# Kernel optimization log

Hardware: AMD Instinct MI355X
Metric: run time of the kernel (lower is better)

## Reference

```python
import jax, jax.numpy as jnp
import numpy as np

N, DIN, E, BLK = 16384, 128, 262144, 2048
H1, DH1, H2, DH2 = 4, 128, 4, 128
D, L, HT, OUT = 128, 5, 4, 2


def _gat(h_in, src, dst, W, a_s, a_d, b, concat):
    # PyG GATConv (eval mode, no dropout): message src->dst, softmax per dst
    H, Dh = a_s.shape
    h = (h_in @ W).reshape(N, H, Dh)
    als = jnp.einsum('nhd,hd->nh', h, a_s)
    ald = jnp.einsum('nhd,hd->nh', h, a_d)
    e = jax.nn.leaky_relu(als[src] + ald[dst], 0.2)            # [E2,H]
    m = jax.ops.segment_max(e, dst, num_segments=N)
    ex = jnp.exp(e - m[dst])
    den = jax.ops.segment_sum(ex, dst, num_segments=N)
    alpha = ex / (den[dst] + 1e-16)
    out = jax.ops.segment_sum(alpha[:, :, None] * h[src], dst, num_segments=N)
    return (out.reshape(N, H * Dh) if concat else out.mean(axis=1)) + b


def _pe():
    pos = jnp.arange(L, dtype=jnp.float32)[:, None]
    div = jnp.exp(jnp.arange(0, D, 2, dtype=jnp.float32) * (-jnp.log(10000.0) / D))
    return jnp.zeros((L, D)).at[:, 0::2].set(jnp.sin(pos * div)).at[:, 1::2].set(jnp.cos(pos * div))


def reference(x, edge_index, time_step, W1, a_src1, a_dst1, b1, W2, a_src2, a_dst2, b2,
              wq, bq, wk, bk, wv, bv, wo, bo, ln_g, ln_b, f1, fb1, f2, fb2, wc, bc):
    s, d = edge_index[0], edge_index[1]
    loops = jnp.arange(N, dtype=edge_index.dtype)
    src = jnp.concatenate([s, d, loops])
    dst = jnp.concatenate([d, s, loops])

    # structural encoder (two GAT layers)
    h = jax.nn.elu(_gat(x, src, dst, W1, a_src1, a_dst1, b1, True))
    h2 = _gat(h, src, dst, W2, a_src2, a_dst2, b2, False)       # [N, D]

    # temporal self-attention: banks are empty (one snapshot per node), so
    # seq has only the last slot valid; original detaches seq before temporal.
    seq = jnp.zeros((N, L, D), h2.dtype).at[:, L - 1].set(jax.lax.stop_gradient(h2))
    xs = seq + _pe()[None]                                       # [N,L,D]
    dh = D // HT
    q = xs[:, -1]                                                # only last query is used
    Q = (q @ wq + bq).reshape(N, HT, dh)
    K = (xs @ wk + bk).reshape(N, L, HT, dh)
    V = (xs @ wv + bv).reshape(N, L, HT, dh)
    scores = jnp.einsum('nhd,nlhd->nhl', Q, K) / jnp.sqrt(jnp.float32(dh))
    valid = (jnp.arange(L) == L - 1)                             # key_padding_mask: pad except last
    scores = jnp.where(valid[None, None, :], scores, -1e9)
    attn = jax.nn.softmax(scores, axis=-1)
    ctx = jnp.einsum('nhl,nlhd->nhd', attn, V).reshape(N, D)
    ao = ctx @ wo + bo

    def ln(v):
        mu = v.mean(-1, keepdims=True)
        var = v.var(-1, keepdims=True)
        return (v - mu) / jnp.sqrt(var + 1e-5) * ln_g + ln_b

    y = ln(q + ao)
    y = ln(y + jax.nn.relu(y @ f1 + fb1) @ f2 + fb2)
    return y @ wc + bc                                           # [N, 2]


def setup_inputs():
    key = jax.random.key(0)
    ks = jax.random.split(key, 20)
    src = jax.random.randint(ks[0], (E,), 0, N, dtype=jnp.int32)
    off = jax.random.randint(ks[1], (E,), 0, BLK, dtype=jnp.int32)
    dst = (src // BLK) * BLK + off                               # within-snapshot edges
    r = lambda k, shape, s=0.05: jax.random.normal(k, shape, jnp.float32) * s
    return {
        'x': jax.random.normal(ks[2], (N, DIN), jnp.float32),
        'edge_index': jnp.stack([src, dst]),
        'time_step': (jnp.arange(N) // BLK).astype(jnp.int64),
        'W1': r(ks[3], (DIN, H1 * DH1)), 'a_src1': r(ks[4], (H1, DH1)), 'a_dst1': r(ks[5], (H1, DH1)), 'b1': jnp.zeros((H1 * DH1,)),
        'W2': r(ks[6], (H1 * DH1, H2 * DH2)), 'a_src2': r(ks[7], (H2, DH2)), 'a_dst2': r(ks[8], (H2, DH2)), 'b2': jnp.zeros((DH2,)),
        'wq': r(ks[9], (D, D)), 'bq': jnp.zeros((D,)), 'wk': r(ks[10], (D, D)), 'bk': jnp.zeros((D,)),
        'wv': r(ks[11], (D, D)), 'bv': jnp.zeros((D,)), 'wo': r(ks[12], (D, D)), 'bo': jnp.zeros((D,)),
        'ln_g': jnp.ones((D,)), 'ln_b': jnp.zeros((D,)),
        'f1': r(ks[13], (D, 4 * D)), 'fb1': jnp.zeros((4 * D,)), 'f2': r(ks[14], (4 * D, D)), 'fb2': jnp.zeros((D,)),
        'wc': r(ks[15], (D, OUT)), 'bc': jnp.zeros((OUT,)),
    }
```

## Files before the change

kernel.cpp:

```cpp
#include <hip/hip_runtime.h>
#include <hip/hip_bf16.h>

#define NODES 16384
#define FEAT 512
typedef __hip_bfloat16 bf16;
typedef __hip_bfloat162 bf162;
typedef short short8v __attribute__((ext_vector_type(8)));
typedef float f32x4 __attribute__((ext_vector_type(4)));

static __device__ __forceinline__ float b2f(short s){
  return __uint_as_float(((unsigned)(unsigned short)s) << 16);
}
static __device__ __forceinline__ void split_store(bf16* h, bf16* l, size_t i, float v){
  bf16 hi = __float2bfloat16(v);
  h[i] = hi; l[i] = __float2bfloat16(v - __bfloat162float(hi));
}

__global__ void sentinel_kernel(float* __restrict__ out, int n, float v){
  int i = blockIdx.x*blockDim.x + threadIdx.x;
  if (i < n) out[i] = v;
}

__global__ void zero_kernel(int* __restrict__ p, int n){
  int i = blockIdx.x*blockDim.x + threadIdx.x;
  if (i < n) p[i] = 0;
}
__global__ void count_kernel(const int* __restrict__ ei, int* __restrict__ counts, int E){
  int i = blockIdx.x*blockDim.x + threadIdx.x;
  if (i < 2*E){
    int dst = (i < E) ? ei[E+i] : ei[i-E];
    atomicAdd(&counts[dst], 1);
  }
}
__global__ __launch_bounds__(1024) void scan_kernel(const int* __restrict__ counts,
                                                    int* __restrict__ offs, int* __restrict__ cursor){
  __shared__ int sh[1024];
  const int t = threadIdx.x;
  int loc[16]; int s = 0;
#pragma unroll
  for (int i=0;i<16;i++){ loc[i] = counts[t*16+i]; s += loc[i]; }
  sh[t] = s; __syncthreads();
  for (int d=1; d<1024; d<<=1){
    int v = (t>=d) ? sh[t-d] : 0;
    __syncthreads(); sh[t] += v; __syncthreads();
  }
  int run = (t==0) ? 0 : sh[t-1];
#pragma unroll
  for (int i=0;i<16;i++){ offs[t*16+i] = run; cursor[t*16+i] = run; run += loc[i]; }
  if (t==1023) offs[NODES] = run;
}
__global__ void fill_kernel(const int* __restrict__ ei, int* __restrict__ cursor,
                            unsigned short* __restrict__ csr, int E){
  int i = blockIdx.x*blockDim.x + threadIdx.x;
  if (i < 2*E){
    int src = ei[i];
    int dst = (i < E) ? ei[E+i] : ei[i-E];
    int pos = atomicAdd(&cursor[dst], 1);
    csr[pos] = (unsigned short)src;
  }
}

struct PrepArgs {
  const float *x,*W1,*W2,*wv,*wo,*f1,*f2;
  bf16 *xh,*w1h,*w2h,*wvh,*wvl,*woh,*wol,*f1h,*f1l,*f2h,*f2l;
};
__global__ __launch_bounds__(256) void prep_kernel(PrepArgs P){
  const int b = blockIdx.x;
  const int t = threadIdx.x;
  if (b < 512){
    const size_t base = (size_t)b*4096;
#pragma unroll
    for (int k=0;k<16;k++){
      const size_t i = base + t + 256*k;
      P.xh[i] = __float2bfloat16(P.x[i]);
    }
    return;
  }
  __shared__ float tile[64][65];
  const float* src; bf16 *dh; bf16 *dl; int R, C, ti;
  int bb = b - 512;
  if (bb < 16){ src=P.W1; dh=P.w1h; dl=nullptr; R=128; C=512; ti=bb; }
  else if ((bb-=16) < 64){ src=P.W2; dh=P.w2h; dl=nullptr; R=512; C=512; ti=bb; }
  else if ((bb-=64) < 4){ src=P.wv; dh=P.wvh; dl=P.wvl; R=128; C=128; ti=bb; }
  else if ((bb-=4) < 4){ src=P.wo; dh=P.woh; dl=P.wol; R=128; C=128; ti=bb; }
  else if ((bb-=4) < 16){ src=P.f1; dh=P.f1h; dl=P.f1l; R=128; C=512; ti=bb; }
  else { bb-=16; src=P.f2; dh=P.f2h; dl=P.f2l; R=512; C=128; ti=bb; }
  const int ctiles = C/64;
  const int r0 = (ti/ctiles)*64, c0 = (ti%ctiles)*64;
  const int r = t >> 6, c = t & 63;
#pragma unroll
  for (int i=0;i<16;i++)
    tile[r + 4*i][c] = src[(size_t)(r0 + r + 4*i)*C + c0 + c];
  __syncthreads();
#pragma unroll
  for (int i=0;i<16;i++){
    const int oc   = c0 + r + 4*i;
    const int orow = r0 + c;
    const float v = tile[c][r + 4*i];
    const size_t oi = (size_t)oc*R + orow;
    if (dl){ split_store(dh, dl, oi, v); } else { dh[oi] = __float2bfloat16(v); }
  }
}

static __device__ __forceinline__ short8v ld8(const bf16* p){
  return *(const short8v*)(const void*)(p);
}

template<int K, int SA, int SB, int ACT, int OMODE, int ALS>
__global__ __launch_bounds__(256) void lgemm(
    const bf16* __restrict__ A, const bf16* __restrict__ Al,
    const bf16* __restrict__ B, const bf16* __restrict__ Bl,
    const float* __restrict__ bias,
    float* __restrict__ Cf, bf16* __restrict__ Ch, bf16* __restrict__ Cl, int N,
    const float* __restrict__ as_p, const float* __restrict__ ad_p,
    float* __restrict__ als_p, float* __restrict__ ald_p){
  __shared__ bf16 As[128*40];
  __shared__ bf16 Bs[128*40];
  __shared__ bf16 Asl[SA ? 128*40 : 1];
  __shared__ bf16 Bsl[SB ? 128*40 : 1];
  const int tid = threadIdx.x;
  const int l = tid & 63, w = tid >> 6;
  const int lg = l >> 4, lr = l & 15;
  const int wr = w >> 1, wc = w & 1;
  const int r0 = blockIdx.x*128;
  const int c0 = blockIdx.y*128;
  const int srow = tid >> 1;
  const int spos = (tid & 1) * 16;
  f32x4 acc[4][4] = {};
  const int ard[4] = { (wr*64 +  0 + lr)*40 + lg*8, (wr*64 + 16 + lr)*40 + lg*8,
                       (wr*64 + 32 + lr)*40 + lg*8, (wr*64 + 48 + lr)*40 + lg*8 };
  const int brd[4] = { (wc*64 +  0 + lr)*40 + lg*8, (wc*64 + 16 + lr)*40 + lg*8,
                       (wc*64 + 32 + lr)*40 + lg*8, (wc*64 + 48 + lr)*40 + lg*8 };
  const size_t agbase = (size_t)(r0 + srow)*K + spos;
  const size_t bgbase = (size_t)(c0 + srow)*K + spos;
  const int sl = srow*40 + spos;
#pragma unroll
  for (int k0 = 0; k0 < K; k0 += 32){
    *(short8v*)&As[sl]     = ld8(A + agbase + k0);
    *(short8v*)&As[sl + 8] = ld8(A + agbase + k0 + 8);
    *(short8v*)&Bs[sl]     = ld8(B + bgbase + k0);
    *(short8v*)&Bs[sl + 8] = ld8(B + bgbase + k0 + 8);
    if (SA){
      *(short8v*)&Asl[sl]     = ld8(Al + agbase + k0);
      *(short8v*)&Asl[sl + 8] = ld8(Al + agbase + k0 + 8);
    }
    if (SB){
      *(short8v*)&Bsl[sl]     = ld8(Bl + bgbase + k0);
      *(short8v*)&Bsl[sl + 8] = ld8(Bl + bgbase + k0 + 8);
    }
    __syncthreads();
    short8v af[4], bfr[4], afl[4], bfl[4];
#pragma unroll
    for (int f=0; f<4; f++){
      af[f]  = *(const short8v*)&As[ard[f]];
      bfr[f] = *(const short8v*)&Bs[brd[f]];
      if (SA) afl[f] = *(const short8v*)&Asl[ard[f]];
      if (SB) bfl[f] = *(const short8v*)&Bsl[brd[f]];
    }
#pragma unroll
    for (int fm=0; fm<4; fm++)
#pragma unroll
      for (int fn=0; fn<4; fn++){
        acc[fm][fn] = __builtin_amdgcn_mfma_f32_16x16x32_bf16(af[fm], bfr[fn], acc[fm][fn], 0,0,0);
        if (SB) acc[fm][fn] = __builtin_amdgcn_mfma_f32_16x16x32_bf16(af[fm], bfl[fn], acc[fm][fn], 0,0,0);
        if (SA) acc[fm][fn] = __builtin_amdgcn_mfma_f32_16x16x32_bf16(afl[fm], bfr[fn], acc[fm][fn], 0,0,0);
      }
    __syncthreads();
  }
  float asv[4], adv[4];
  float rs[4][4], rd[4][4];
  if (ALS){
#pragma unroll
    for (int fn=0; fn<4; fn++){
      const int col = c0 + wc*64 + fn*16 + lr;
      asv[fn] = as_p[col]; adv[fn] = ad_p[col];
    }
#pragma unroll
    for (int fm=0; fm<4; fm++)
#pragma unroll
      for (int r=0; r<4; r++){ rs[fm][r] = 0.f; rd[fm][r] = 0.f; }
  }
#pragma unroll
  for (int fm=0; fm<4; fm++){
#pragma unroll
    for (int fn=0; fn<4; fn++){
      const int col = c0 + wc*64 + fn*16 + lr;
      const float bv = bias ? bias[col] : 0.f;
#pragma unroll
      for (int r=0; r<4; r++){
        const int row = r0 + wr*64 + fm*16 + lg*4 + r;
        float v = acc[fm][fn][r] + bv;
        if (ACT==1) v = fmaxf(v, 0.f);
        const size_t idx = (size_t)row*N + col;
        if (OMODE==0) Cf[idx] = v;
        else if (OMODE==1){
          bf16 bvv = __float2bfloat16(v);
          Ch[idx] = bvv;
          if (ALS){
            const float hv = __bfloat162float(bvv);
            rs[fm][r] += hv*asv[fn];
            rd[fm][r] += hv*adv[fn];
          }
        }
        else split_store(Ch, Cl, idx, v);
      }
    }
  }
  if (ALS){
    float* rb = (float*)As;
#pragma unroll
    for (int fm=0; fm<4; fm++)
#pragma unroll
      for (int r=0; r<4; r++){
        float s = rs[fm][r], dd = rd[fm][r];
#pragma unroll
        for (int mask=1; mask<16; mask<<=1){
          s  += __shfl_xor(s,  mask);
          dd += __shfl_xor(dd, mask);
        }
        rs[fm][r] = s; rd[fm][r] = dd;
      }
    if (wc == 1 && lr == 0){
#pragma unroll
      for (int fm=0; fm<4; fm++)
#pragma unroll
        for (int r=0; r<4; r++){
          const int row = wr*64 + fm*16 + lg*4 + r;
          rb[row] = rs[fm][r]; rb[128+row] = rd[fm][r];
        }
    }
    __syncthreads();
    if (wc == 0 && lr == 0){
      const int head = blockIdx.y;
#pragma unroll
      for (int fm=0; fm<4; fm++)
#pragma unroll
        for (int r=0; r<4; r++){
          const int row = wr*64 + fm*16 + lg*4 + r;
          als_p[(size_t)(r0+row)*4 + head] = rs[fm][r] + rb[row];
          ald_p[(size_t)(r0+row)*4 + head] = rd[fm][r] + rb[128+row];
        }
    }
  }
}

template<bool CONCAT>
__global__ __launch_bounds__(256) void gat_fused_kernel(const bf16* __restrict__ hfeat,
    const float* __restrict__ als, const float* __restrict__ ald,
    const int* __restrict__ offs, const unsigned short* __restrict__ csr,
    const float* __restrict__ bias, void* __restrict__ outv,
    bf16* __restrict__ qh, bf16* __restrict__ ql){
  const int w = threadIdx.x >> 6, l = threadIdx.x & 63, g = l >> 4, s16 = l & 15;
  const int nb = blockIdx.x;
  const int n = (nb & 7)*2048 + (nb >> 3)*4 + w;
  const float adg = ald[(size_t)n*4 + g];
  const int beg = offs[n];
  const int cnt = offs[n+1] - beg + 1;
  float ev[6]; int sv[6];
#pragma unroll
  for (int p=0;p<6;p++){
    const int i = s16 + p*16;
    int src = n;
    float e = -1e30f;
    if (i < cnt){
      if (i < cnt-1) src = (int)csr[beg+i];
      float t = als[(size_t)src*4+g] + adg;
      e = fmaxf(t, 0.2f*t);
    }
    ev[p] = e; sv[p] = src;
  }
  float m = -1e30f;
#pragma unroll
  for (int p=0;p<6;p++) m = fmaxf(m, ev[p]);
  float den = 0.f;
#pragma unroll
  for (int p=0;p<6;p++) den += (ev[p] > -1e29f) ? __expf(ev[p]-m) : 0.f;
#pragma unroll
  for (int mask=1; mask<16; mask<<=1){
    float mo = __shfl_xor(m, mask);
    float dd = __shfl_xor(den, mask);
    float nm = fmaxf(m, mo);
    den = den*__expf(m-nm) + dd*__expf(mo-nm);
    m = nm;
  }
  const float C = __expf(-m)/(den + 1e-16f);
  int pk[6];
#pragma unroll
  for (int p=0;p<6;p++){
    float a = (ev[p] > -1e29f) ? __expf(ev[p])*C : 0.f;
    bf16 ab = __float2bfloat16(a);
    pk[p] = ((int)*(unsigned short*)&ab << 16) | (sv[p] & 0xFFFF);
  }
  float acc[8] = {0,0,0,0,0,0,0,0};
  const int fb = l*8;
  const bf16* hp = hfeat + fb;
#pragma unroll
  for (int p=0;p<6;p++){
    const int pbase = p*16;
    if (pbase < cnt){
      const int lim = (cnt - pbase < 16) ? (cnt - pbase) : 16;
      int u_c = __shfl(pk[p], (l & 48));
      short8v hv_c = *(const short8v*)(const void*)(hp + (size_t)(u_c & 0xFFFF)*FEAT);
      for (int j=1; j<lim; ++j){
        const int u_n = __shfl(pk[p], (l & 48) | j);
        const short8v hv_n = *(const short8v*)(const void*)(hp + (size_t)(u_n & 0xFFFF)*FEAT);
        const float a_c = __uint_as_float((unsigned)u_c & 0xFFFF0000u);
#pragma unroll
        for (int k=0;k<8;k++) acc[k] += a_c * b2f(hv_c[k]);
        u_c = u_n; hv_c = hv_n;
      }
      const float a_c = __uint_as_float((unsigned)u_c & 0xFFFF0000u);
#pragma unroll
      for (int k=0;k<8;k++) acc[k] += a_c * b2f(hv_c[k]);
    }
  }
  for (int i = 96; i < cnt; ++i){
    const int src = (i < cnt-1) ? (int)csr[beg+i] : n;
    float t = als[(size_t)src*4+g] + adg;
    t = fmaxf(t, 0.2f*t);
    const float a = __expf(t)*C;
    const short8v hv = *(const short8v*)(const void*)&hfeat[(size_t)src*FEAT + fb];
#pragma unroll
    for (int k=0;k<8;k++) acc[k] += a * b2f(hv[k]);
  }
  if (CONCAT){
    short8v ov;
#pragma unroll
    for (int j=0;j<8;j++){
      float v = acc[j] + bias[fb+j];
      v = v > 0.f ? v : expm1f(v);
      bf16 bv = __float2bfloat16(v);
      ov[j] = (short)*(unsigned short*)&bv;
    }
    *(short8v*)((char*)outv + ((size_t)n*FEAT + fb)*2) = ov;
  } else {
#pragma unroll
    for (int j=0;j<8;j++){
      acc[j] += __shfl_xor(acc[j], 16);
      acc[j] += __shfl_xor(acc[j], 32);
    }
    if (l < 16){
      float* op = (float*)outv + (size_t)n*128 + l*8;
#pragma unroll
      for (int j=0;j<8;j++){
        const int col = l*8 + j;
        float v = 0.25f*acc[j] + bias[col];
        float ex = __expf((float)(col & ~1) * (-9.210340371976184f/128.f));
        float pe = (col & 1) ? cosf(4.f*ex) : sinf(4.f*ex);
        float q = v + pe;
        op[j] = q;
        split_store(qh, ql, (size_t)n*128 + col, q);
      }
    }
  }
}

template<int SPLIT>
__global__ __launch_bounds__(256) void ln_kernel(const float* __restrict__ a, const float* __restrict__ b,
    const float* __restrict__ g, const float* __restrict__ bb, float* __restrict__ out,
    bf16* __restrict__ oh, bf16* __restrict__ ol){
  int row = blockIdx.x*4 + (threadIdx.x >> 6);
  int lane = threadIdx.x & 63;
  int c = lane*2;
  float2 va = *(const float2*)&a[(size_t)row*128 + c];
  float2 vb = *(const float2*)&b[(size_t)row*128 + c];
  float x0 = va.x+vb.x, x1 = va.y+vb.y;
  float s = x0+x1, q = x0*x0 + x1*x1;
#pragma unroll
  for (int o=32;o>0;o>>=1){ s += __shfl_xor(s,o); q += __shfl_xor(q,o); }
  float mu = s*(1.f/128.f);
  float var = q*(1.f/128.f) - mu*mu;
  float r = 1.f/sqrtf(var + 1e-5f);
  float y0 = (x0-mu)*r*g[c]   + bb[c];
  float y1 = (x1-mu)*r*g[c+1] + bb[c+1];
  size_t idx = (size_t)row*128 + c;
  out[idx] = y0; out[idx+1] = y1;
  if (SPLIT){ split_store(oh, ol, idx, y0); split_store(oh, ol, idx+1, y1); }
}

__global__ __launch_bounds__(256) void ln_final_kernel(const float* __restrict__ a, const float* __restrict__ b,
    const float* __restrict__ g, const float* __restrict__ bb,
    const float* __restrict__ wc, const float* __restrict__ bc,
    float* __restrict__ out){
  int row = blockIdx.x*4 + (threadIdx.x >> 6);
  int lane = threadIdx.x & 63;
  int c = lane*2;
  float2 va = *(const float2*)&a[(size_t)row*128 + c];
  float2 vb = *(const float2*)&b[(size_t)row*128 + c];
  float x0 = va.x+vb.x, x1 = va.y+vb.y;
  float s = x0+x1, q = x0*x0 + x1*x1;
#pragma unroll
  for (int o=32;o>0;o>>=1){ s += __shfl_xor(s,o); q += __shfl_xor(q,o); }
  float mu = s*(1.f/128.f);
  float var = q*(1.f/128.f) - mu*mu;
  float r = 1.f/sqrtf(var + 1e-5f);
  float y0 = (x0-mu)*r*g[c]   + bb[c];
  float y1 = (x1-mu)*r*g[c+1] + bb[c+1];
  float s0 = y0*wc[c*2]   + y1*wc[(c+1)*2];
  float s1 = y0*wc[c*2+1] + y1*wc[(c+1)*2+1];
#pragma unroll
  for (int o=32;o>0;o>>=1){ s0 += __shfl_xor(s0,o); s1 += __shfl_xor(s1,o); }
  if (lane == 0){
    out[row*2]   = s0 + bc[0];
    out[row*2+1] = s1 + bc[1];
  }
}

extern "C" void kernel_launch(void* const* d_in, const int* in_sizes, int n_in,
                              void* d_out, int out_size, void* d_ws, size_t ws_size,
                              hipStream_t stream){
  const float* x      = (const float*)d_in[0];
  const int*   ei     = (const int*)d_in[1];
  const float* W1     = (const float*)d_in[3];
  const float* a_src1 = (const float*)d_in[4];
  const float* a_dst1 = (const float*)d_in[5];
  const float* b1     = (const float*)d_in[6];
  const float* W2     = (const float*)d_in[7];
  const float* a_src2 = (const float*)d_in[8];
  const float* a_dst2 = (const float*)d_in[9];
  const float* b2     = (const float*)d_in[10];
  const float* wv     = (const float*)d_in[15];
  const float* bv     = (const float*)d_in[16];
  const float* wo     = (const float*)d_in[17];
  const float* bo     = (const float*)d_in[18];
  const float* ln_g   = (const float*)d_in[19];
  const float* ln_b   = (const float*)d_in[20];
  const float* f1     = (const float*)d_in[21];
  const float* fb1    = (const float*)d_in[22];
  const float* f2     = (const float*)d_in[23];
  const float* fb2    = (const float*)d_in[24];
  const float* wc     = (const float*)d_in[25];
  const float* bc     = (const float*)d_in[26];
  float* outp = (float*)d_out;

  const int E = in_sizes[1] / 2;
  const int n = NODES;
  const int tE = 2*E;
  const size_t MB = 1024*1024;

  const size_t NEED = 36*MB;
  if (ws_size < NEED){
    sentinel_kernel<<<(out_size+255)/256, 256, 0, stream>>>(outp, out_size,
        1000.0f + (float)(ws_size / MB));
    return;
  }

  char* base = (char*)d_ws;
  int* counts = (int*)(base + 0);
  int* cursor = (int*)(base + 65536);
  bf16*  h1    = (bf16*)(base + 0);
  bf16*  xh    = (bf16*)(base + 16*MB);
  bf16*  h     = (bf16*)(base + 16*MB);
  bf16*  h2f   = (bf16*)(base + 0);
  float* h2q   = (float*)(base + 16*MB);
  bf16*  qh    = (bf16*)(base + 24*MB);
  bf16*  ql    = (bf16*)(base + 28*MB);
  bf16*  vh    = (bf16*)(base + 0);
  bf16*  vl    = (bf16*)(base + 4*MB);
  float* aobuf = (float*)(base + 8*MB);
  float* y1    = (float*)(base + 24*MB);
  bf16*  y1h   = (bf16*)(base + 0);
  bf16*  y1l   = (bf16*)(base + 4*MB);
  bf16*  hidden= (bf16*)(base + 8*MB);
  float* ffn2f = (float*)(base + 0);
  char* u = base + 32*MB;
  bf16* w1h = (bf16*)u; u += 131072;
  bf16* w2h = (bf16*)u; u += 524288;
  bf16* wvh = (bf16*)u; u += 32768;   bf16* wvl = (bf16*)u; u += 32768;
  bf16* woh = (bf16*)u; u += 32768;   bf16* wol = (bf16*)u; u += 32768;
  bf16* f1h = (bf16*)u; u += 131072;  bf16* f1l = (bf16*)u; u += 131072;
  bf16* f2h = (bf16*)u; u += 131072;  bf16* f2l = (bf16*)u; u += 131072;
  float* als  = (float*)u; u += (size_t)n*4*4;
  float* ald  = (float*)u; u += (size_t)n*4*4;
  int* offs   = (int*)u;   u += (size_t)(n+1)*4 + 252;
  unsigned short* csr = (unsigned short*)u; u += (size_t)tE*2;

  PrepArgs P = { x,W1,W2,wv,wo,f1,f2, xh,w1h,w2h,wvh,wvl,woh,wol,f1h,f1l,f2h,f2l };
  prep_kernel<<<632, 256, 0, stream>>>(P);
  zero_kernel<<<(n+255)/256, 256, 0, stream>>>(counts, n);
  count_kernel<<<(tE+255)/256, 256, 0, stream>>>(ei, counts, E);
  scan_kernel<<<1, 1024, 0, stream>>>(counts, offs, cursor);
  fill_kernel<<<(tE+255)/256, 256, 0, stream>>>(ei, cursor, csr, E);

  lgemm<128,0,0,0,1,1><<<dim3(128,4), 256, 0, stream>>>(xh, nullptr, w1h, nullptr, nullptr,
      nullptr, h1, nullptr, 512, a_src1, a_dst1, als, ald);
  gat_fused_kernel<true><<<n/4, 256, 0, stream>>>(h1, als, ald, offs, csr, b1, h, nullptr, nullptr);

  lgemm<512,0,0,0,1,1><<<dim3(128,4), 256, 0, stream>>>(h, nullptr, w2h, nullptr, nullptr,
      nullptr, h2f, nullptr, 512, a_src2, a_dst2, als, ald);
  gat_fused_kernel<false><<<n/4, 256, 0, stream>>>(h2f, als, ald, offs, csr, b2, h2q, qh, ql);

  lgemm<128,1,1,0,2,0><<<dim3(128,1), 256, 0, stream>>>(qh, ql, wvh, wvl, bv,
      nullptr, vh, vl, 128, nullptr, nullptr, nullptr, nullptr);
  lgemm<128,1,1,0,0,0><<<dim3(128,1), 256, 0, stream>>>(vh, vl, woh, wol, bo,
      aobuf, nullptr, nullptr, 128, nullptr, nullptr, nullptr, nullptr);
  ln_kernel<1><<<n/4, 256, 0, stream>>>(h2q, aobuf, ln_g, ln_b, y1, y1h, y1l);
  lgemm<128,1,1,1,1,0><<<dim3(128,4), 256, 0, stream>>>(y1h, y1l, f1h, f1l, fb1,
      nullptr, hidden, nullptr, 512, nullptr, nullptr, nullptr, nullptr);
  lgemm<512,0,1,0,0,0><<<dim3(128,1), 256, 0, stream>>>(hidden, nullptr, f2h, f2l, fb2,
      ffn2f, nullptr, nullptr, 128, nullptr, nullptr, nullptr, nullptr);
  ln_final_kernel<<<n/4, 256, 0, stream>>>(y1, ffn2f, ln_g, ln_b, wc, bc, outp);
}
```

Before: 264.2 us.

## Fuse residual LayerNorm and classifier head into GEMM epilogues

Adds an LNM mode to the GEMM epilogue. The Wo GEMM now adds the residual, applies LayerNorm and writes y1 (fp32 and split bf16). The FFN2 GEMM now adds the residual, applies LayerNorm and the 2-wide classifier, then writes the final output. This removes two standalone LayerNorm kernels and the fp32 aobuf/ffn2f round trips through global memory. It also rewrites the GAT gather to unpack bf16 pairs from 32-bit words. The cost is more registers and LDS cross-wave reductions in the epilogue, with only 128 blocks for the fused N=128 GEMMs.

```diff
diff --git a/kernel.cpp b/kernel.cpp
--- a/kernel.cpp
+++ b/kernel.cpp
@@ -6,6 +6,7 @@
 typedef __hip_bfloat16 bf16;
 typedef __hip_bfloat162 bf162;
 typedef short short8v __attribute__((ext_vector_type(8)));
+typedef unsigned int uint4v __attribute__((ext_vector_type(4)));
 typedef float f32x4 __attribute__((ext_vector_type(4)));
 
 static __device__ __forceinline__ float b2f(short s){
@@ -106,14 +107,17 @@
   return *(const short8v*)(const void*)(p);
 }
 
-template<int K, int SA, int SB, int ACT, int OMODE, int ALS>
+template<int K, int SA, int SB, int ACT, int OMODE, int ALS, int LNM>
 __global__ __launch_bounds__(256) void lgemm(
     const bf16* __restrict__ A, const bf16* __restrict__ Al,
     const bf16* __restrict__ B, const bf16* __restrict__ Bl,
     const float* __restrict__ bias,
     float* __restrict__ Cf, bf16* __restrict__ Ch, bf16* __restrict__ Cl, int N,
     const float* __restrict__ as_p, const float* __restrict__ ad_p,
-    float* __restrict__ als_p, float* __restrict__ ald_p){
+    float* __restrict__ als_p, float* __restrict__ ald_p,
+    const float* __restrict__ qbuf, const float* __restrict__ lng, const float* __restrict__ lnb,
+    float* __restrict__ y1f, bf16* __restrict__ y1ho, bf16* __restrict__ y1lo,
+    const float* __restrict__ wcp, const float* __restrict__ bcp, float* __restrict__ outp){
   __shared__ bf16 As[128*40];
   __shared__ bf16 Bs[128*40];
   __shared__ bf16 Asl[SA ? 128*40 : 1];
@@ -167,79 +171,210 @@
       }
     __syncthreads();
   }
-  float asv[4], adv[4];
-  float rs[4][4], rd[4][4];
-  if (ALS){
-#pragma unroll
-    for (int fn=0; fn<4; fn++){
-      const int col = c0 + wc*64 + fn*16 + lr;
-      asv[fn] = as_p[col]; adv[fn] = ad_p[col];
-    }
+  if (LNM == 0){
+    float asv[4], adv[4];
+    float rs[4][4], rd[4][4];
+    if (ALS){
+#pragma unroll
+      for (int fn=0; fn<4; fn++){
+        const int col = c0 + wc*64 + fn*16 + lr;
+        asv[fn] = as_p[col]; adv[fn] = ad_p[col];
+      }
+#pragma unroll
+      for (int fm=0; fm<4; fm++)
+#pragma unroll
+        for (int r=0; r<4; r++){ rs[fm][r] = 0.f; rd[fm][r] = 0.f; }
+    }
+#pragma unroll
+    for (int fm=0; fm<4; fm++){
+#pragma unroll
+      for (int fn=0; fn<4; fn++){
+        const int col = c0 + wc*64 + fn*16 + lr;
+        const float bv = bias ? bias[col] : 0.f;
+#pragma unroll
+        for (int r=0; r<4; r++){
+          const int row = r0 + wr*64 + fm*16 + lg*4 + r;
+          float v = acc[fm][fn][r] + bv;
+          if (ACT==1) v = fmaxf(v, 0.f);
+          const size_t idx = (size_t)row*N + col;
+          if (OMODE==0) Cf[idx] = v;
+          else if (OMODE==1){
+            bf16 bvv = __float2bfloat16(v);
+            Ch[idx] = bvv;
+            if (ALS){
+              const float hv = __bfloat162float(bvv);
+              rs[fm][r] += hv*asv[fn];
+              rd[fm][r] += hv*adv[fn];
+            }
+          }
+          else split_store(Ch, Cl, idx, v);
+        }
+      }
+    }
+    if (ALS){
+      float* rb = (float*)As;
+#pragma unroll
+      for (int fm=0; fm<4; fm++)
+#pragma unroll
+        for (int r=0; r<4; r++){
+          float s = rs[fm][r], dd = rd[fm][r];
+#pragma unroll
+          for (int mask=1; mask<16; mask<<=1){
+            s  += __shfl_xor(s,  mask);
+            dd += __shfl_xor(dd, mask);
+          }
+          rs[fm][r] = s; rd[fm][r] = dd;
+        }
+      if (wc == 1 && lr == 0){
+#pragma unroll
+        for (int fm=0; fm<4; fm++)
+#pragma unroll
+          for (int r=0; r<4; r++){
+            const int row = wr*64 + fm*16 + lg*4 + r;
+            rb[row] = rs[fm][r]; rb[128+row] = rd[fm][r];
+          }
+      }
+      __syncthreads();
+      if (wc == 0 && lr == 0){
+        const int head = blockIdx.y;
+#pragma unroll
+        for (int fm=0; fm<4; fm++)
+#pragma unroll
+          for (int r=0; r<4; r++){
+            const int row = wr*64 + fm*16 + lg*4 + r;
+            als_p[(size_t)(r0+row)*4 + head] = rs[fm][r] + rb[row];
+            ald_p[(size_t)(r0+row)*4 + head] = rd[fm][r] + rb[128+row];
+          }
+      }
+    }
+  } else {
+    float s1[4][4], s2[4][4];
 #pragma unroll
     for (int fm=0; fm<4; fm++)
 #pragma unroll
-      for (int r=0; r<4; r++){ rs[fm][r] = 0.f; rd[fm][r] = 0.f; }
-  }
-#pragma unroll
-  for (int fm=0; fm<4; fm++){
-#pragma unroll
-    for (int fn=0; fn<4; fn++){
-      const int col = c0 + wc*64 + fn*16 + lr;
-      const float bv = bias ? bias[col] : 0.f;
+      for (int r=0; r<4; r++){ s1[fm][r] = 0.f; s2[fm][r] = 0.f; }
+#pragma unroll
+    for (int fm=0; fm<4; fm++)
+#pragma unroll
+      for (int fn=0; fn<4; fn++){
+        const int col = wc*64 + fn*16 + lr;
+        const float bv = bias[col];
+#pragma unroll
+        for (int r=0; r<4; r++){
+          const int row = r0 + wr*64 + fm*16 + lg*4 + r;
+          float xx = qbuf[(size_t)row*128 + col] + acc[fm][fn][r] + bv;
+          acc[fm][fn][r] = xx;
+          s1[fm][r] += xx;
+          s2[fm][r] += xx*xx;
+        }
+      }
+    float* rb = (float*)As;
+#pragma unroll
+    for (int fm=0; fm<4; fm++)
 #pragma unroll
       for (int r=0; r<4; r++){
-        const int row = r0 + wr*64 + fm*16 + lg*4 + r;
-        float v = acc[fm][fn][r] + bv;
-        if (ACT==1) v = fmaxf(v, 0.f);
-        const size_t idx = (size_t)row*N + col;
-        if (OMODE==0) Cf[idx] = v;
-        else if (OMODE==1){
-          bf16 bvv = __float2bfloat16(v);
-          Ch[idx] = bvv;
-          if (ALS){
-            const float hv = __bfloat162float(bvv);
-            rs[fm][r] += hv*asv[fn];
-            rd[fm][r] += hv*adv[fn];
-          }
-        }
-        else split_store(Ch, Cl, idx, v);
-      }
-    }
-  }
-  if (ALS){
-    float* rb = (float*)As;
-#pragma unroll
-    for (int fm=0; fm<4; fm++)
-#pragma unroll
-      for (int r=0; r<4; r++){
-        float s = rs[fm][r], dd = rd[fm][r];
+        float a = s1[fm][r], b = s2[fm][r];
 #pragma unroll
         for (int mask=1; mask<16; mask<<=1){
-          s  += __shfl_xor(s,  mask);
-          dd += __shfl_xor(dd, mask);
-        }
-        rs[fm][r] = s; rd[fm][r] = dd;
-      }
-    if (wc == 1 && lr == 0){
+          a += __shfl_xor(a, mask);
+          b += __shfl_xor(b, mask);
+        }
+        s1[fm][r] = a; s2[fm][r] = b;
+      }
+    if (lr == 0){
 #pragma unroll
       for (int fm=0; fm<4; fm++)
 #pragma unroll
         for (int r=0; r<4; r++){
           const int row = wr*64 + fm*16 + lg*4 + r;
-          rb[row] = rs[fm][r]; rb[128+row] = rd[fm][r];
+          rb[row*4 + wc*2 + 0] = s1[fm][r];
+          rb[row*4 + wc*2 + 1] = s2[fm][r];
         }
     }
     __syncthreads();
-    if (wc == 0 && lr == 0){
-      const int head = blockIdx.y;
+    float mu[4][4], ri[4][4];
+#pragma unroll
+    for (int fm=0; fm<4; fm++)
+#pragma unroll
+      for (int r=0; r<4; r++){
+        const int row = wr*64 + fm*16 + lg*4 + r;
+        const float st  = s1[fm][r] + rb[row*4 + (wc^1)*2 + 0];
+        const float s2t = s2[fm][r] + rb[row*4 + (wc^1)*2 + 1];
+        const float m  = st*(1.f/128.f);
+        const float va = s2t*(1.f/128.f) - m*m;
+        mu[fm][r] = m;
+        ri[fm][r] = 1.f/sqrtf(va + 1e-5f);
+      }
+    if (LNM == 1){
+#pragma unroll
+      for (int fm=0; fm<4; fm++)
+#pragma unroll
+        for (int fn=0; fn<4; fn++){
+          const int col = wc*64 + fn*16 + lr;
+          const float gv = lng[col], bbv = lnb[col];
+#pragma unroll
+          for (int r=0; r<4; r++){
+            const int row = r0 + wr*64 + fm*16 + lg*4 + r;
+            const float ln = (acc[fm][fn][r] - mu[fm][r])*ri[fm][r]*gv + bbv;
+            const size_t idx = (size_t)row*128 + col;
+            y1f[idx] = ln;
+            split_store(y1ho, y1lo, idx, ln);
+          }
+        }
+    } else {
+      float p0[4][4], p1[4][4];
+#pragma unroll
+      for (int fm=0; fm<4; fm++)
+#pragma unroll
+        for (int r=0; r<4; r++){ p0[fm][r] = 0.f; p1[fm][r] = 0.f; }
+#pragma unroll
+      for (int fm=0; fm<4; fm++)
+#pragma unroll
+        for (int fn=0; fn<4; fn++){
+          const int col = wc*64 + fn*16 + lr;
+          const float gv = lng[col], bbv = lnb[col];
+          const float w0 = wcp[col*2], w1 = wcp[col*2+1];
+#pragma unroll
+          for (int r=0; r<4; r++){
+            const float ln = (acc[fm][fn][r] - mu[fm][r])*ri[fm][r]*gv + bbv;
+            p0[fm][r] += ln*w0;
+            p1[fm][r] += ln*w1;
+          }
+        }
+      __syncthreads();
 #pragma unroll
       for (int fm=0; fm<4; fm++)
 #pragma unroll
         for (int r=0; r<4; r++){
-          const int row = wr*64 + fm*16 + lg*4 + r;
-          als_p[(size_t)(r0+row)*4 + head] = rs[fm][r] + rb[row];
-          ald_p[(size_t)(r0+row)*4 + head] = rd[fm][r] + rb[128+row];
-        }
+          float a = p0[fm][r], b = p1[fm][r];
+#pragma unroll
+          for (int mask=1; mask<16; mask<<=1){
+            a += __shfl_xor(a, mask);
+            b += __shfl_xor(b, mask);
+          }
+          p0[fm][r] = a; p1[fm][r] = b;
+        }
+      if (lr == 0){
+#pragma unroll
+        for (int fm=0; fm<4; fm++)
+#pragma unroll
+          for (int r=0; r<4; r++){
+            const int row = wr*64 + fm*16 + lg*4 + r;
+            rb[row*4 + wc*2 + 0] = p0[fm][r];
+            rb[row*4 + wc*2 + 1] = p1[fm][r];
+          }
+      }
+      __syncthreads();
+      if (wc == 0 && lr == 0){
+#pragma unroll
+        for (int fm=0; fm<4; fm++)
+#pragma unroll
+          for (int r=0; r<4; r++){
+            const int row = wr*64 + fm*16 + lg*4 + r;
+            outp[(size_t)(r0+row)*2 + 0] = p0[fm][r] + rb[row*4 + 2] + bcp[0];
+            outp[(size_t)(r0+row)*2 + 1] = p1[fm][r] + rb[row*4 + 3] + bcp[1];
+          }
+      }
     }
   }
 }
@@ -300,18 +435,24 @@
     if (pbase < cnt){
       const int lim = (cnt - pbase < 16) ? (cnt - pbase) : 16;
       int u_c = __shfl(pk[p], (l & 48));
-      short8v hv_c = *(const short8v*)(const void*)(hp + (size_t)(u_c & 0xFFFF)*FEAT);
+      uint4v hv_c = *(const uint4v*)(const void*)(hp + (size_t)(u_c & 0xFFFF)*FEAT);
       for (int j=1; j<lim; ++j){
         const int u_n = __shfl(pk[p], (l & 48) | j);
-        const short8v hv_n = *(const short8v*)(const void*)(hp + (size_t)(u_n & 0xFFFF)*FEAT);
+        const uint4v hv_n = *(const uint4v*)(const void*)(hp + (size_t)(u_n & 0xFFFF)*FEAT);
         const float a_c = __uint_as_float((unsigned)u_c & 0xFFFF0000u);
 #pragma unroll
-        for (int k=0;k<8;k++) acc[k] += a_c * b2f(hv_c[k]);
+        for (int k=0;k<4;k++){
+          acc[2*k]   += a_c * __uint_as_float(hv_c[k] << 16);
+          acc[2*k+1] += a_c * __uint_as_float(hv_c[k] & 0xFFFF0000u);
+        }
         u_c = u_n; hv_c = hv_n;
       }
       const float a_c = __uint_as_float((unsigned)u_c & 0xFFFF0000u);
 #pragma unroll
-      for (int k=0;k<8;k++) acc[k] += a_c * b2f(hv_c[k]);
+      for (int k=0;k<4;k++){
+        acc[2*k]   += a_c * __uint_as_float(hv_c[k] << 16);
+        acc[2*k+1] += a_c * __uint_as_float(hv_c[k] & 0xFFFF0000u);
+      }
     }
   }
   for (int i = 96; i < cnt; ++i){
@@ -352,57 +493,6 @@
         split_store(qh, ql, (size_t)n*128 + col, q);
       }
     }
-  }
-}
-
-template<int SPLIT>
-__global__ __launch_bounds__(256) void ln_kernel(const float* __restrict__ a, const float* __restrict__ b,
-    const float* __restrict__ g, const float* __restrict__ bb, float* __restrict__ out,
-    bf16* __restrict__ oh, bf16* __restrict__ ol){
-  int row = blockIdx.x*4 + (threadIdx.x >> 6);
-  int lane = threadIdx.x & 63;
-  int c = lane*2;
-  float2 va = *(const float2*)&a[(size_t)row*128 + c];
-  float2 vb = *(const float2*)&b[(size_t)row*128 + c];
-  float x0 = va.x+vb.x, x1 = va.y+vb.y;
-  float s = x0+x1, q = x0*x0 + x1*x1;
-#pragma unroll
-  for (int o=32;o>0;o>>=1){ s += __shfl_xor(s,o); q += __shfl_xor(q,o); }
-  float mu = s*(1.f/128.f);
-  float var = q*(1.f/128.f) - mu*mu;
-  float r = 1.f/sqrtf(var + 1e-5f);
-  float y0 = (x0-mu)*r*g[c]   + bb[c];
-  float y1 = (x1-mu)*r*g[c+1] + bb[c+1];
-  size_t idx = (size_t)row*128 + c;
-  out[idx] = y0; out[idx+1] = y1;
-  if (SPLIT){ split_store(oh, ol, idx, y0); split_store(oh, ol, idx+1, y1); }
-}
-
-__global__ __launch_bounds__(256) void ln_final_kernel(const float* __restrict__ a, const float* __restrict__ b,
-    const float* __restrict__ g, const float* __restrict__ bb,
-    const float* __restrict__ wc, const float* __restrict__ bc,
-    float* __restrict__ out){
-  int row = blockIdx.x*4 + (threadIdx.x >> 6);
-  int lane = threadIdx.x & 63;
-  int c = lane*2;
-  float2 va = *(const float2*)&a[(size_t)row*128 + c];
-  float2 vb = *(const float2*)&b[(size_t)row*128 + c];
-  float x0 = va.x+vb.x, x1 = va.y+vb.y;
-  float s = x0+x1, q = x0*x0 + x1*x1;
-#pragma unroll
-  for (int o=32;o>0;o>>=1){ s += __shfl_xor(s,o); q += __shfl_xor(q,o); }
-  float mu = s*(1.f/128.f);
-  float var = q*(1.f/128.f) - mu*mu;
-  float r = 1.f/sqrtf(var + 1e-5f);
-  float y0 = (x0-mu)*r*g[c]   + bb[c];
-  float y1 = (x1-mu)*r*g[c+1] + bb[c+1];
-  float s0 = y0*wc[c*2]   + y1*wc[(c+1)*2];
-  float s1 = y0*wc[c*2+1] + y1*wc[(c+1)*2+1];
-#pragma unroll
-  for (int o=32;o>0;o>>=1){ s0 += __shfl_xor(s0,o); s1 += __shfl_xor(s1,o); }
-  if (lane == 0){
-    out[row*2]   = s0 + bc[0];
-    out[row*2+1] = s1 + bc[1];
   }
 }
 
@@ -457,12 +547,10 @@
   bf16*  ql    = (bf16*)(base + 28*MB);
   bf16*  vh    = (bf16*)(base + 0);
   bf16*  vl    = (bf16*)(base + 4*MB);
-  float* aobuf = (float*)(base + 8*MB);
   float* y1    = (float*)(base + 24*MB);
   bf16*  y1h   = (bf16*)(base + 0);
   bf16*  y1l   = (bf16*)(base + 4*MB);
   bf16*  hidden= (bf16*)(base + 8*MB);
-  float* ffn2f = (float*)(base + 0);
   char* u = base + 32*MB;
   bf16* w1h = (bf16*)u; u += 131072;
   bf16* w2h = (bf16*)u; u += 524288;
@@ -482,22 +570,26 @@
   scan_kernel<<<1, 1024, 0, stream>>>(counts, offs, cursor);
   fill_kernel<<<(tE+255)/256, 256, 0, stream>>>(ei, cursor, csr, E);
 
-  lgemm<128,0,0,0,1,1><<<dim3(128,4), 256, 0, stream>>>(xh, nullptr, w1h, nullptr, nullptr,
-      nullptr, h1, nullptr, 512, a_src1, a_dst1, als, ald);
+  lgemm<128,0,0,0,1,1,0><<<dim3(128,4), 256, 0, stream>>>(xh, nullptr, w1h, nullptr, nullptr,
+      nullptr, h1, nullptr, 512, a_src1, a_dst1, als, ald,
+      nullptr,nullptr,nullptr,nullptr,nullptr,nullptr,nullptr,nullptr,nullptr);
   gat_fused_kernel<true><<<n/4, 256, 0, stream>>>(h1, als, ald, offs, csr, b1, h, nullptr, nullptr);
 
-  lgemm<512,0,0,0,1,1><<<dim3(128,4), 256, 0, stream>>>(h, nullptr, w2h, nullptr, nullptr,
-      nullptr, h2f, nullptr, 512, a_src2, a_dst2, als, ald);
+  lgemm<512,0,0,0,1,1,0><<<dim3(128,4), 256, 0, stream>>>(h, nullptr, w2h, nullptr, nullptr,
+      nullptr, h2f, nullptr, 512, a_src2, a_dst2, als, ald,
+      nullptr,nullptr,nullptr,nullptr,nullptr,nullptr,nullptr,nullptr,nullptr);
   gat_fused_kernel<false><<<n/4, 256, 0, stream>>>(h2f, als, ald, offs, csr, b2, h2q, qh, ql);
 
-  lgemm<128,1,1,0,2,0><<<dim3(128,1), 256, 0, stream>>>(qh, ql, wvh, wvl, bv,
-      nullptr, vh, vl, 128, nullptr, nullptr, nullptr, nullptr);
-  lgemm<128,1,1,0,0,0><<<dim3(128,1), 256, 0, stream>>>(vh, vl, woh, wol, bo,
-      aobuf, nullptr, nullptr, 128, nullptr, nullptr, nullptr, nullptr);
-  ln_kernel<1><<<n/4, 256, 0, stream>>>(h2q, aobuf, ln_g, ln_b, y1, y1h, y1l);
-  lgemm<128,1,1,1,1,0><<<dim3(128,4), 256, 0, stream>>>(y1h, y1l, f1h, f1l, fb1,
-      nullptr, hidden, nullptr, 512, nullptr, nullptr, nullptr, nullptr);
-  lgemm<512,0,1,0,0,0><<<dim3(128,1), 256, 0, stream>>>(hidden, nullptr, f2h, f2l, fb2,
-      ffn2f, nullptr, nullptr, 128, nullptr, nullptr, nullptr, nullptr);
-  ln_final_kernel<<<n/4, 256, 0, stream>>>(y1, ffn2f, ln_g, ln_b, wc, bc, outp);
-}
+  lgemm<128,1,1,0,2,0,0><<<dim3(128,1), 256, 0, stream>>>(qh, ql, wvh, wvl, bv,
+      nullptr, vh, vl, 128, nullptr, nullptr, nullptr, nullptr,
+      nullptr,nullptr,nullptr,nullptr,nullptr,nullptr,nullptr,nullptr,nullptr);
+  lgemm<128,1,1,0,0,0,1><<<dim3(128,1), 256, 0, stream>>>(vh, vl, woh, wol, bo,
+      nullptr, nullptr, nullptr, 128, nullptr, nullptr, nullptr, nullptr,
+      h2q, ln_g, ln_b, y1, y1h, y1l, nullptr, nullptr, nullptr);
+  lgemm<128,1,1,1,1,0,0><<<dim3(128,4), 256, 0, stream>>>(y1h, y1l, f1h, f1l, fb1,
+      nullptr, hidden, nullptr, 512, nullptr, nullptr, nullptr, nullptr,
+      nullptr,nullptr,nullptr,nullptr,nullptr,nullptr,nullptr,nullptr,nullptr);
+  lgemm<512,0,1,0,0,0,2><<<dim3(128,1), 256, 0, stream>>>(hidden, nullptr, f2h, f2l, fb2,
+      nullptr, nullptr, nullptr, 128, nullptr, nullptr, nullptr, nullptr,
+      y1, ln_g, ln_b, nullptr, nullptr, nullptr, wc, bc, outp);
+}
```

Result: faster. 252.9 us (-4.3%).
